# Kernel optimization log

Measured on AMD Instinct MI355X. Metric: run time of the kernel, lower is better.

The kernel has to match this reference:

```python
import jax, jax.numpy as jnp
import numpy as np

N_NODES = 100000
N_EDGES = 1600000
IN_DIM = 64
OUT_DIM = 64
T_STEPS = 4
W_SCALE = 0.01


def setup_inputs() -> dict:
    key = jax.random.key(0)
    k0, k1, k2, k3, k4, k5 = jax.random.split(key, 6)
    Xv = jax.random.normal(k0, (N_NODES, IN_DIM), dtype=jnp.float32)
    edge_index = jax.random.randint(k1, (2, N_EDGES), 0, N_NODES, dtype=jnp.int64)
    W1 = jax.random.normal(k2, (OUT_DIM, IN_DIM), dtype=jnp.float32) * W_SCALE
    W2 = jax.random.normal(k3, (OUT_DIM, OUT_DIM), dtype=jnp.float32) * W_SCALE
    W3 = jax.random.normal(k4, (OUT_DIM, OUT_DIM), dtype=jnp.float32) * W_SCALE
    W4 = jax.random.normal(k5, (OUT_DIM, 1), dtype=jnp.float32) * W_SCALE
    return {"Xv": Xv, "edge_index": edge_index, "W1": W1, "W2": W2, "W3": W3, "W4": W4}


def reference(Xv, edge_index, W1, W2, W3, W4):
    n = Xv.shape[0]
    row = edge_index[0]
    col = edge_index[1]
    # Dense A (all-ones COO, duplicates summed) passed through W4 -> ReLU -> sum over axis 1:
    # sum_j relu(A_ij * w4) = sum_j A_ij * relu(w4)  (ReLU is positively homogeneous, A_ij >= 0)
    #                       = deg_i * relu(w4)
    deg = jax.ops.segment_sum(jnp.ones(row.shape, Xv.dtype), row, num_segments=n)  # [N]
    w4 = W4[:, 0]  # [D]
    v3 = (deg[:, None] * jax.nn.relu(w4)[None, :]) @ W3.T  # [N, D]
    base = Xv @ W1.T + v3  # loop-invariant part (recomputed each step in original, same value)
    emb = jnp.zeros((n, W1.shape[0]), Xv.dtype)
    for _ in range(T_STEPS):
        # sparse A @ emb: gather source embeddings, scatter-add into destination rows
        neigh = jax.ops.segment_sum(emb[col], row, num_segments=n)  # [N, D]
        emb = jax.nn.relu(base + neigh @ W2.T)
    return emb
```

## Files before the change

kernel.cpp:

```cpp
#include <hip/hip_runtime.h>

#define NN 100000
#define NE 1600000
#define D  64
#define BSH 8
#define NBKT ((NN + 255) >> BSH)
#define NBLK_E ((NE / 4 + 1023) / 1024)
#define H_SCALE 256.0f
#define H_ISCALE 0.00390625f

typedef __attribute__((ext_vector_type(8))) short short8v;
typedef __attribute__((ext_vector_type(4))) unsigned short ushort4v;
typedef __attribute__((ext_vector_type(4))) float f32x4;
typedef __attribute__((ext_vector_type(2))) float f32x2;

__device__ __forceinline__ float bf2f(unsigned short x) {
    return __uint_as_float(((unsigned)x) << 16);
}
__device__ __forceinline__ unsigned short f2bf(float f) {
    unsigned u = __float_as_uint(f);
    return (unsigned short)((u + 0x7fff + ((u >> 16) & 1)) >> 16);
}

__global__ __launch_bounds__(256) void k_prep(
        const float* __restrict__ W1, const float* __restrict__ W2,
        const float* __restrict__ W3, const float* __restrict__ W4,
        unsigned short* __restrict__ w1b, unsigned short* __restrict__ w2b,
        float* __restrict__ cvec, int* __restrict__ ghist) {
    int b = blockIdx.x, tid = threadIdx.x;
    if (b < 16) {
        int i = b * 256 + tid;
        w1b[i] = f2bf(W1[i]);
        w2b[i] = f2bf(W2[i]);
    } else {
        for (int i = tid; i < NBKT; i += 256) ghist[i] = 0;
        if (tid < 64) {
            float s = 0.f;
            for (int k = 0; k < D; ++k) {
                float w4 = W4[k];
                s += W3[tid * D + k] * (w4 > 0.f ? w4 : 0.f);
            }
            cvec[tid] = s;
        }
    }
}

__global__ __launch_bounds__(256) void k_hist(const int* __restrict__ row,
                                              int* __restrict__ ghist) {
    __shared__ int h[NBKT];
    int tid = threadIdx.x;
    for (int i = tid; i < NBKT; i += 256) h[i] = 0;
    __syncthreads();
    int base4 = blockIdx.x * 1024;
    #pragma unroll
    for (int k = 0; k < 4; ++k) {
        int i4 = base4 + k * 256 + tid;
        if (i4 < NE / 4) {
            int4 r = ((const int4*)row)[i4];
            atomicAdd(&h[r.x >> BSH], 1);
            atomicAdd(&h[r.y >> BSH], 1);
            atomicAdd(&h[r.z >> BSH], 1);
            atomicAdd(&h[r.w >> BSH], 1);
        }
    }
    __syncthreads();
    for (int i = tid; i < NBKT; i += 256) if (h[i]) atomicAdd(&ghist[i], h[i]);
}

__global__ __launch_bounds__(256) void k_bscan(const int* __restrict__ ghist,
                                               int* __restrict__ bbase,
                                               int* __restrict__ bcur) {
    __shared__ int sc[2][512];
    int t = threadIdx.x;
    int cur = 0;
    #pragma unroll
    for (int k = 0; k < 2; ++k) {
        int i = t + k * 256;
        sc[0][i] = (i < NBKT) ? ghist[i] : 0;
    }
    __syncthreads();
    for (int s = 1; s < 512; s <<= 1) {
        #pragma unroll
        for (int k = 0; k < 2; ++k) {
            int i = t + k * 256;
            sc[cur ^ 1][i] = sc[cur][i] + ((i >= s) ? sc[cur][i - s] : 0);
        }
        cur ^= 1;
        __syncthreads();
    }
    #pragma unroll
    for (int k = 0; k < 2; ++k) {
        int i = t + k * 256;
        if (i < NBKT) {
            int b = (i == 0) ? 0 : sc[cur][i - 1];
            bbase[i] = b;
            bcur[i] = b;
        } else if (i == NBKT) {
            bbase[NBKT] = sc[cur][NBKT - 1];
        }
    }
}

__global__ __launch_bounds__(256) void k_bucket(const int* __restrict__ row,
                                                const int* __restrict__ col,
                                                int* __restrict__ bcur,
                                                unsigned* __restrict__ sorted) {
    __shared__ int hist[NBKT];
    __shared__ int bbase_s[NBKT];
    int tid = threadIdx.x;
    for (int i = tid; i < NBKT; i += 256) hist[i] = 0;
    __syncthreads();
    int base4 = blockIdx.x * 1024;
    int4 r4[4], c4[4];
    int rank[16];
    bool valid[4];
    #pragma unroll
    for (int k = 0; k < 4; ++k) {
        int i4 = base4 + k * 256 + tid;
        valid[k] = (i4 < NE / 4);
        if (valid[k]) {
            r4[k] = ((const int4*)row)[i4];
            c4[k] = ((const int4*)col)[i4];
            rank[k * 4 + 0] = atomicAdd(&hist[r4[k].x >> BSH], 1);
            rank[k * 4 + 1] = atomicAdd(&hist[r4[k].y >> BSH], 1);
            rank[k * 4 + 2] = atomicAdd(&hist[r4[k].z >> BSH], 1);
            rank[k * 4 + 3] = atomicAdd(&hist[r4[k].w >> BSH], 1);
        }
    }
    __syncthreads();
    for (int i = tid; i < NBKT; i += 256)
        bbase_s[i] = hist[i] ? atomicAdd(&bcur[i], hist[i]) : 0;
    __syncthreads();
    #pragma unroll
    for (int k = 0; k < 4; ++k) {
        if (valid[k]) {
            int rr[4] = {r4[k].x, r4[k].y, r4[k].z, r4[k].w};
            int cc[4] = {c4[k].x, c4[k].y, c4[k].z, c4[k].w};
            #pragma unroll
            for (int j = 0; j < 4; ++j) {
                int b = rr[j] >> BSH;
                unsigned pk = ((unsigned)(rr[j] & 255) << 17) | (unsigned)cc[j];
                sorted[bbase_s[b] + rank[k * 4 + j]] = pk;
            }
        }
    }
}

__global__ __launch_bounds__(256) void k_fine(const unsigned* __restrict__ sorted,
                                              const int* __restrict__ bbase,
                                              int* __restrict__ csr_col,
                                              int* __restrict__ cnt_g,
                                              int2* __restrict__ se_g) {
    __shared__ int cnt_s[256];
    __shared__ int cur_s[256];
    __shared__ int sc[2][256];
    int b = blockIdx.x;
    int tid = threadIdx.x;
    int s0 = bbase[b], e0 = bbase[b + 1];
    cnt_s[tid] = 0;
    __syncthreads();
    for (int i = s0 + tid; i < e0; i += 256)
        atomicAdd(&cnt_s[sorted[i] >> 17], 1);
    __syncthreads();
    int cur = 0;
    sc[0][tid] = cnt_s[tid];
    __syncthreads();
    for (int s = 1; s < 256; s <<= 1) {
        sc[cur ^ 1][tid] = sc[cur][tid] + ((tid >= s) ? sc[cur][tid - s] : 0);
        cur ^= 1;
        __syncthreads();
    }
    int incl = sc[cur][tid];
    cur_s[tid] = incl - cnt_s[tid];
    int nb = NN - b * 256;
    nb = nb > 256 ? 256 : nb;
    if (tid < nb) {
        int node = b * 256 + tid;
        cnt_g[node] = cnt_s[tid];
        se_g[node] = make_int2(s0 + incl - cnt_s[tid], s0 + incl);
    }
    __syncthreads();
    for (int i = s0 + tid; i < e0; i += 256) {
        unsigned u = sorted[i];
        int p = atomicAdd(&cur_s[u >> 17], 1);
        csr_col[s0 + p] = (int)(u & 0x1FFFFu);
    }
}

__global__ __launch_bounds__(256) void k_baseh(
        const float* __restrict__ Xv, const unsigned short* __restrict__ w1b,
        const unsigned short* __restrict__ w2b,
        const int* __restrict__ cnt, const float* __restrict__ cvec,
        unsigned short* __restrict__ base_bf, unsigned char* __restrict__ h8) {
    __shared__ unsigned short etile[4][16][72];
    int wv = threadIdx.x >> 6;
    int wid = blockIdx.x * 4 + wv;
    int lane = threadIdx.x & 63;
    int m0 = wid * 16;
    if (m0 >= NN) return;
    int r = lane & 15, half = lane >> 4;
    const float* arow = Xv + (size_t)(m0 + r) * D + half * 8;
    f32x4 xa = *(const f32x4*)(arow);
    f32x4 xb = *(const f32x4*)(arow + 4);
    f32x4 xc = *(const f32x4*)(arow + 32);
    f32x4 xd = *(const f32x4*)(arow + 36);
    short8v a0, a1;
    #pragma unroll
    for (int j = 0; j < 4; ++j) {
        a0[j]     = (short)f2bf(xa[j]);
        a0[j + 4] = (short)f2bf(xb[j]);
        a1[j]     = (short)f2bf(xc[j]);
        a1[j + 4] = (short)f2bf(xd[j]);
    }
    int4 c4 = *(const int4*)(cnt + m0 + half * 4);
    float dg[4] = {(float)c4.x, (float)c4.y, (float)c4.z, (float)c4.w};
    #pragma unroll
    for (int t = 0; t < 4; ++t) {
        short8v b0 = *(const short8v*)(w1b + (size_t)(t * 16 + r) * D + half * 8);
        short8v b1 = *(const short8v*)(w1b + (size_t)(t * 16 + r) * D + 32 + half * 8);
        f32x4 cacc = {0.f, 0.f, 0.f, 0.f};
        cacc = __builtin_amdgcn_mfma_f32_16x16x32_bf16(a0, b0, cacc, 0, 0, 0);
        cacc = __builtin_amdgcn_mfma_f32_16x16x32_bf16(a1, b1, cacc, 0, 0, 0);
        float cv = cvec[t * 16 + r];
        #pragma unroll
        for (int q = 0; q < 4; ++q) {
            float s = cacc[q] + dg[q] * cv;
            size_t idx = (size_t)(m0 + half * 4 + q) * D + t * 16 + r;
            base_bf[idx] = f2bf(s);
            etile[wv][half * 4 + q][t * 16 + r] = f2bf(s > 0.f ? s : 0.f);
        }
    }
    short8v ha0 = *(const short8v*)(&etile[wv][r][half * 8]);
    short8v ha1 = *(const short8v*)(&etile[wv][r][32 + half * 8]);
    #pragma unroll
    for (int t = 0; t < 4; ++t) {
        short8v b0 = *(const short8v*)(w2b + (size_t)(t * 16 + r) * D + half * 8);
        short8v b1 = *(const short8v*)(w2b + (size_t)(t * 16 + r) * D + 32 + half * 8);
        f32x4 cacc = {0.f, 0.f, 0.f, 0.f};
        cacc = __builtin_amdgcn_mfma_f32_16x16x32_bf16(ha0, b0, cacc, 0, 0, 0);
        cacc = __builtin_amdgcn_mfma_f32_16x16x32_bf16(ha1, b1, cacc, 0, 0, 0);
        #pragma unroll
        for (int q = 0; q < 4; ++q) {
            int pk = __builtin_amdgcn_cvt_pk_fp8_f32(cacc[q] * H_SCALE, 0.f, 0, false);
            h8[(size_t)(m0 + half * 4 + q) * D + t * 16 + r] = (unsigned char)(pk & 0xff);
        }
    }
}

template<int LAST>
__global__ __launch_bounds__(256) void k_pullh(
        const int2* __restrict__ se_g,
        const int* __restrict__ csr_col, const unsigned char* __restrict__ h_in,
        const unsigned short* __restrict__ base_bf,
        const unsigned short* __restrict__ w2b,
        unsigned char* __restrict__ h_out, float* __restrict__ out_f32) {
    __shared__ unsigned short etile[16][72];
    int tid = threadIdx.x;
    int wv = tid >> 6, lane = tid & 63;
    int q = lane >> 4, l = lane & 15;
    int m0 = blockIdx.x * 16;
    #pragma unroll
    for (int s = 0; s < 4; ++s) {
        int node = m0 + wv * 4 + s;
        int2 se = se_g[node];
        int start = se.x, end = se.y;
        float a0 = 0.f, a1 = 0.f, a2 = 0.f, a3 = 0.f;
        for (int j = start; j < end; j += 16) {
            int e0 = j + q;
            int e1 = j + 4 + q;
            int e2 = j + 8 + q;
            int e3 = j + 12 + q;
            int c0 = (e0 < end) ? csr_col[e0] : -1;
            int c1 = (e1 < end) ? csr_col[e1] : -1;
            int c2 = (e2 < end) ? csr_col[e2] : -1;
            int c3 = (e3 < end) ? csr_col[e3] : -1;
            unsigned v0 = 0, v1 = 0, v2 = 0, v3 = 0;
            if (c0 >= 0) v0 = *((const unsigned*)(h_in + (size_t)c0 * D) + l);
            if (c1 >= 0) v1 = *((const unsigned*)(h_in + (size_t)c1 * D) + l);
            if (c2 >= 0) v2 = *((const unsigned*)(h_in + (size_t)c2 * D) + l);
            if (c3 >= 0) v3 = *((const unsigned*)(h_in + (size_t)c3 * D) + l);
            if (c0 >= 0) {
                f32x2 f0 = __builtin_amdgcn_cvt_pk_f32_fp8(v0, false);
                f32x2 f1 = __builtin_amdgcn_cvt_pk_f32_fp8(v0, true);
                a0 += f0.x; a1 += f0.y; a2 += f1.x; a3 += f1.y;
            }
            if (c1 >= 0) {
                f32x2 f0 = __builtin_amdgcn_cvt_pk_f32_fp8(v1, false);
                f32x2 f1 = __builtin_amdgcn_cvt_pk_f32_fp8(v1, true);
                a0 += f0.x; a1 += f0.y; a2 += f1.x; a3 += f1.y;
            }
            if (c2 >= 0) {
                f32x2 f0 = __builtin_amdgcn_cvt_pk_f32_fp8(v2, false);
                f32x2 f1 = __builtin_amdgcn_cvt_pk_f32_fp8(v2, true);
                a0 += f0.x; a1 += f0.y; a2 += f1.x; a3 += f1.y;
            }
            if (c3 >= 0) {
                f32x2 f0 = __builtin_amdgcn_cvt_pk_f32_fp8(v3, false);
                f32x2 f1 = __builtin_amdgcn_cvt_pk_f32_fp8(v3, true);
                a0 += f0.x; a1 += f0.y; a2 += f1.x; a3 += f1.y;
            }
        }
        a0 += __shfl_xor(a0, 16); a1 += __shfl_xor(a1, 16);
        a2 += __shfl_xor(a2, 16); a3 += __shfl_xor(a3, 16);
        a0 += __shfl_xor(a0, 32); a1 += __shfl_xor(a1, 32);
        a2 += __shfl_xor(a2, 32); a3 += __shfl_xor(a3, 32);
        ushort4v b4 = *(const ushort4v*)(base_bf + (size_t)node * D + l * 4);
        float r0 = fmaxf(fmaf(a0, H_ISCALE, bf2f(b4[0])), 0.f);
        float r1 = fmaxf(fmaf(a1, H_ISCALE, bf2f(b4[1])), 0.f);
        float r2 = fmaxf(fmaf(a2, H_ISCALE, bf2f(b4[2])), 0.f);
        float r3 = fmaxf(fmaf(a3, H_ISCALE, bf2f(b4[3])), 0.f);
        if (LAST) {
            if (q == 0) {
                f32x4 o4 = {r0, r1, r2, r3};
                *(f32x4*)(out_f32 + (size_t)node * D + l * 4) = o4;
            }
        } else {
            if (q == 0) {
                ushort4v o4 = {f2bf(r0), f2bf(r1), f2bf(r2), f2bf(r3)};
                *(ushort4v*)(&etile[wv * 4 + s][l * 4]) = o4;
            }
        }
    }
    if (!LAST) {
        __syncthreads();
        int r = lane & 15, half = lane >> 4;
        short8v ha0 = *(const short8v*)(&etile[r][half * 8]);
        short8v ha1 = *(const short8v*)(&etile[r][32 + half * 8]);
        int t = wv;
        short8v b0 = *(const short8v*)(w2b + (size_t)(t * 16 + r) * D + half * 8);
        short8v b1 = *(const short8v*)(w2b + (size_t)(t * 16 + r) * D + 32 + half * 8);
        f32x4 cacc = {0.f, 0.f, 0.f, 0.f};
        cacc = __builtin_amdgcn_mfma_f32_16x16x32_bf16(ha0, b0, cacc, 0, 0, 0);
        cacc = __builtin_amdgcn_mfma_f32_16x16x32_bf16(ha1, b1, cacc, 0, 0, 0);
        #pragma unroll
        for (int qq = 0; qq < 4; ++qq) {
            int pk = __builtin_amdgcn_cvt_pk_fp8_f32(cacc[qq] * H_SCALE, 0.f, 0, false);
            h_out[(size_t)(m0 + half * 4 + qq) * D + t * 16 + r] = (unsigned char)(pk & 0xff);
        }
    }
}

extern "C" void kernel_launch(void* const* d_in, const int* in_sizes, int n_in,
                              void* d_out, int out_size, void* d_ws, size_t ws_size,
                              hipStream_t stream) {
    const float* Xv = (const float*)d_in[0];
    const int*   ei = (const int*)d_in[1];
    const float* W1 = (const float*)d_in[2];
    const float* W2 = (const float*)d_in[3];
    const float* W3 = (const float*)d_in[4];
    const float* W4 = (const float*)d_in[5];

    char* ws = (char*)d_ws;
    size_t off = 0;
    unsigned short* base_bf = (unsigned short*)(ws + off); off += (size_t)NN * D * 2;
    unsigned char* h8a = (unsigned char*)(ws + off);   off += (size_t)NN * D;
    unsigned char* h8b = (unsigned char*)(ws + off);   off += (size_t)NN * D;
    int* csr_col = (int*)(ws + off);                   off += (size_t)NE * 4;
    int* cnt     = (int*)(ws + off);                   off += (size_t)NN * 4;
    int2* se_g   = (int2*)(ws + off);                  off += (size_t)NN * 8;
    int* ghist   = (int*)(ws + off);                   off += NBKT * 4;
    int* bbase   = (int*)(ws + off);                   off += (NBKT + 1) * 4;
    int* bcur    = (int*)(ws + off);                   off += NBKT * 4;
    float* cvec  = (float*)(ws + off);                 off += D * 4;
    unsigned short* w1b = (unsigned short*)(ws + off); off += D * D * 2;
    unsigned short* w2b = (unsigned short*)(ws + off); off += D * D * 2;
    unsigned* sorted = (unsigned*)(ws + off);          off += (size_t)NE * 4;

    float* emb_f32 = (float*)d_out;

    const int* row = ei;
    const int* col = ei + NE;

    k_prep<<<17, 256, 0, stream>>>(W1, W2, W3, W4, w1b, w2b, cvec, ghist);
    k_hist<<<NBLK_E, 256, 0, stream>>>(row, ghist);
    k_bscan<<<1, 256, 0, stream>>>(ghist, bbase, bcur);
    k_bucket<<<NBLK_E, 256, 0, stream>>>(row, col, bcur, sorted);
    k_fine<<<NBKT, 256, 0, stream>>>(sorted, bbase, csr_col, cnt, se_g);

    k_baseh<<<(NN / 16 + 3) / 4, 256, 0, stream>>>(Xv, w1b, w2b, cnt, cvec,
                                                   base_bf, h8a);

    k_pullh<0><<<NN / 16, 256, 0, stream>>>(se_g, csr_col, h8a, base_bf, w2b, h8b, nullptr);
    k_pullh<0><<<NN / 16, 256, 0, stream>>>(se_g, csr_col, h8b, base_bf, w2b, h8a, nullptr);
    k_pullh<1><<<NN / 16, 256, 0, stream>>>(se_g, csr_col, h8a, base_bf, w2b, nullptr, emb_f32);
}
```

Baseline: 201.2 us.

## Pad CSR rows to 4-aligned offsets and vectorize column index loads

The fine CSR build now pads each node's edge segment to a multiple of four, with extra per-bucket slack, so every row starts on a 16-byte boundary. The pull kernel then reads four column indices with a single int4 load in the full-chunk loop and drops the per-edge bounds checks, keeping a guarded tail loop for the remainder. The base load and ReLU epilogue now run only in q==0 lanes. This costs a larger csr_col buffer, and the padding slots must never be read as real edges.

Measured after the change: 193.3 us. 1.04x faster.

```diff
diff --git a/kernel.cpp b/kernel.cpp
--- a/kernel.cpp
+++ b/kernel.cpp
@@ -157,13 +157,16 @@
     int b = blockIdx.x;
     int tid = threadIdx.x;
     int s0 = bbase[b], e0 = bbase[b + 1];
+    int pbase = ((s0 + 3) & ~3) + 768 * b;
     cnt_s[tid] = 0;
     __syncthreads();
     for (int i = s0 + tid; i < e0; i += 256)
         atomicAdd(&cnt_s[sorted[i] >> 17], 1);
     __syncthreads();
+    int cnt = cnt_s[tid];
+    int pc = (cnt + 3) & ~3;
     int cur = 0;
-    sc[0][tid] = cnt_s[tid];
+    sc[0][tid] = pc;
     __syncthreads();
     for (int s = 1; s < 256; s <<= 1) {
         sc[cur ^ 1][tid] = sc[cur][tid] + ((tid >= s) ? sc[cur][tid - s] : 0);
@@ -171,19 +174,20 @@
         __syncthreads();
     }
     int incl = sc[cur][tid];
-    cur_s[tid] = incl - cnt_s[tid];
+    int excl = incl - pc;
+    cur_s[tid] = excl;
     int nb = NN - b * 256;
     nb = nb > 256 ? 256 : nb;
     if (tid < nb) {
         int node = b * 256 + tid;
-        cnt_g[node] = cnt_s[tid];
-        se_g[node] = make_int2(s0 + incl - cnt_s[tid], s0 + incl);
+        cnt_g[node] = cnt;
+        se_g[node] = make_int2(pbase + excl, pbase + excl + cnt);
     }
     __syncthreads();
     for (int i = s0 + tid; i < e0; i += 256) {
         unsigned u = sorted[i];
         int p = atomicAdd(&cur_s[u >> 17], 1);
-        csr_col[s0 + p] = (int)(u & 0x1FFFFu);
+        csr_col[pbase + p] = (int)(u & 0x1FFFFu);
     }
 }
 
@@ -265,7 +269,24 @@
         int2 se = se_g[node];
         int start = se.x, end = se.y;
         float a0 = 0.f, a1 = 0.f, a2 = 0.f, a3 = 0.f;
-        for (int j = start; j < end; j += 16) {
+        int j = start;
+        for (; j + 16 <= end; j += 16) {
+            int4 c = *(const int4*)(csr_col + j + 4 * q);
+            unsigned v0 = *((const unsigned*)(h_in + (size_t)c.x * D) + l);
+            unsigned v1 = *((const unsigned*)(h_in + (size_t)c.y * D) + l);
+            unsigned v2 = *((const unsigned*)(h_in + (size_t)c.z * D) + l);
+            unsigned v3 = *((const unsigned*)(h_in + (size_t)c.w * D) + l);
+            f32x2 f;
+            f = __builtin_amdgcn_cvt_pk_f32_fp8(v0, false); a0 += f.x; a1 += f.y;
+            f = __builtin_amdgcn_cvt_pk_f32_fp8(v0, true);  a2 += f.x; a3 += f.y;
+            f = __builtin_amdgcn_cvt_pk_f32_fp8(v1, false); a0 += f.x; a1 += f.y;
+            f = __builtin_amdgcn_cvt_pk_f32_fp8(v1, true);  a2 += f.x; a3 += f.y;
+            f = __builtin_amdgcn_cvt_pk_f32_fp8(v2, false); a0 += f.x; a1 += f.y;
+            f = __builtin_amdgcn_cvt_pk_f32_fp8(v2, true);  a2 += f.x; a3 += f.y;
+            f = __builtin_amdgcn_cvt_pk_f32_fp8(v3, false); a0 += f.x; a1 += f.y;
+            f = __builtin_amdgcn_cvt_pk_f32_fp8(v3, true);  a2 += f.x; a3 += f.y;
+        }
+        if (j < end) {
             int e0 = j + q;
             int e1 = j + 4 + q;
             int e2 = j + 8 + q;
@@ -279,43 +300,38 @@
             if (c1 >= 0) v1 = *((const unsigned*)(h_in + (size_t)c1 * D) + l);
             if (c2 >= 0) v2 = *((const unsigned*)(h_in + (size_t)c2 * D) + l);
             if (c3 >= 0) v3 = *((const unsigned*)(h_in + (size_t)c3 * D) + l);
+            f32x2 f;
             if (c0 >= 0) {
-                f32x2 f0 = __builtin_amdgcn_cvt_pk_f32_fp8(v0, false);
-                f32x2 f1 = __builtin_amdgcn_cvt_pk_f32_fp8(v0, true);
-                a0 += f0.x; a1 += f0.y; a2 += f1.x; a3 += f1.y;
+                f = __builtin_amdgcn_cvt_pk_f32_fp8(v0, false); a0 += f.x; a1 += f.y;
+                f = __builtin_amdgcn_cvt_pk_f32_fp8(v0, true);  a2 += f.x; a3 += f.y;
             }
             if (c1 >= 0) {
-                f32x2 f0 = __builtin_amdgcn_cvt_pk_f32_fp8(v1, false);
-                f32x2 f1 = __builtin_amdgcn_cvt_pk_f32_fp8(v1, true);
-                a0 += f0.x; a1 += f0.y; a2 += f1.x; a3 += f1.y;
+                f = __builtin_amdgcn_cvt_pk_f32_fp8(v1, false); a0 += f.x; a1 += f.y;
+                f = __builtin_amdgcn_cvt_pk_f32_fp8(v1, true);  a2 += f.x; a3 += f.y;
             }
             if (c2 >= 0) {
-                f32x2 f0 = __builtin_amdgcn_cvt_pk_f32_fp8(v2, false);
-                f32x2 f1 = __builtin_amdgcn_cvt_pk_f32_fp8(v2, true);
-                a0 += f0.x; a1 += f0.y; a2 += f1.x; a3 += f1.y;
+                f = __builtin_amdgcn_cvt_pk_f32_fp8(v2, false); a0 += f.x; a1 += f.y;
+                f = __builtin_amdgcn_cvt_pk_f32_fp8(v2, true);  a2 += f.x; a3 += f.y;
             }
             if (c3 >= 0) {
-                f32x2 f0 = __builtin_amdgcn_cvt_pk_f32_fp8(v3, false);
-                f32x2 f1 = __builtin_amdgcn_cvt_pk_f32_fp8(v3, true);
-                a0 += f0.x; a1 += f0.y; a2 += f1.x; a3 += f1.y;
+                f = __builtin_amdgcn_cvt_pk_f32_fp8(v3, false); a0 += f.x; a1 += f.y;
+                f = __builtin_amdgcn_cvt_pk_f32_fp8(v3, true);  a2 += f.x; a3 += f.y;
             }
         }
         a0 += __shfl_xor(a0, 16); a1 += __shfl_xor(a1, 16);
         a2 += __shfl_xor(a2, 16); a3 += __shfl_xor(a3, 16);
         a0 += __shfl_xor(a0, 32); a1 += __shfl_xor(a1, 32);
         a2 += __shfl_xor(a2, 32); a3 += __shfl_xor(a3, 32);
-        ushort4v b4 = *(const ushort4v*)(base_bf + (size_t)node * D + l * 4);
-        float r0 = fmaxf(fmaf(a0, H_ISCALE, bf2f(b4[0])), 0.f);
-        float r1 = fmaxf(fmaf(a1, H_ISCALE, bf2f(b4[1])), 0.f);
-        float r2 = fmaxf(fmaf(a2, H_ISCALE, bf2f(b4[2])), 0.f);
-        float r3 = fmaxf(fmaf(a3, H_ISCALE, bf2f(b4[3])), 0.f);
-        if (LAST) {
-            if (q == 0) {
+        if (q == 0) {
+            ushort4v b4 = *(const ushort4v*)(base_bf + (size_t)node * D + l * 4);
+            float r0 = fmaxf(fmaf(a0, H_ISCALE, bf2f(b4[0])), 0.f);
+            float r1 = fmaxf(fmaf(a1, H_ISCALE, bf2f(b4[1])), 0.f);
+            float r2 = fmaxf(fmaf(a2, H_ISCALE, bf2f(b4[2])), 0.f);
+            float r3 = fmaxf(fmaf(a3, H_ISCALE, bf2f(b4[3])), 0.f);
+            if (LAST) {
                 f32x4 o4 = {r0, r1, r2, r3};
                 *(f32x4*)(out_f32 + (size_t)node * D + l * 4) = o4;
-            }
-        } else {
-            if (q == 0) {
+            } else {
                 ushort4v o4 = {f2bf(r0), f2bf(r1), f2bf(r2), f2bf(r3)};
                 *(ushort4v*)(&etile[wv * 4 + s][l * 4]) = o4;
             }
@@ -355,7 +371,7 @@
     unsigned short* base_bf = (unsigned short*)(ws + off); off += (size_t)NN * D * 2;
     unsigned char* h8a = (unsigned char*)(ws + off);   off += (size_t)NN * D;
     unsigned char* h8b = (unsigned char*)(ws + off);   off += (size_t)NN * D;
-    int* csr_col = (int*)(ws + off);                   off += (size_t)NE * 4;
+    int* csr_col = (int*)(ws + off);                   off += ((size_t)NE + 768 * NBKT + 16) * 4;
     int* cnt     = (int*)(ws + off);                   off += (size_t)NN * 4;
     int2* se_g   = (int2*)(ws + off);                  off += (size_t)NN * 8;
     int* ghist   = (int*)(ws + off);                   off += NBKT * 4;
@@ -364,6 +380,7 @@
     float* cvec  = (float*)(ws + off);                 off += D * 4;
     unsigned short* w1b = (unsigned short*)(ws + off); off += D * D * 2;
     unsigned short* w2b = (unsigned short*)(ws + off); off += D * D * 2;
+    off = (off + 15) & ~(size_t)15;
     unsigned* sorted = (unsigned*)(ws + off);          off += (size_t)NE * 4;
 
     float* emb_f32 = (float*)d_out;
```
